# Performance work log

Hardware: AMD Instinct MI355X
Metric: run time of the kernel (lower is better)

Reference implementation:

```python
import jax, jax.numpy as jnp
import numpy as np

VOCAB = 50257
HIDDEN = 2048
BATCH = 8
SEQ = 2048
TOPK = 256


def setup_inputs() -> dict:
    key = jax.random.key(0)
    k1, k2 = jax.random.split(key)
    input_ids = jax.random.randint(k1, (BATCH, SEQ), 0, VOCAB, dtype=jnp.int64)
    W = jax.random.normal(k2, (VOCAB, HIDDEN), dtype=jnp.float32)
    return {"input_ids": input_ids, "W": W, "k": TOPK}


def reference(input_ids, W, k):
    # Embedding gather: [B, S] ids -> [B, S, H] logits (irregular row gather).
    logits = jnp.take(W, input_ids, axis=0)
    # Top-k over the last (hidden) dim, sorted descending (matches torch.topk).
    values, indices = jax.lax.top_k(logits, k)
    return values, indices.astype(jnp.int32)
```

## Files before the change

### kernel.cpp

```cpp
#include <hip/hip_runtime.h>
#include <stdint.h>

#define VOCAB  50257
#define HIDDEN 2048
#define NTOK   (8 * 2048)
#define TOPK   256
#define WPB    4


__device__ __forceinline__ void cmpex(uint64_t& a, uint64_t& b, bool desc) {
    bool gt = a > b;
    uint64_t mx = gt ? a : b;
    uint64_t mn = gt ? b : a;
    a = desc ? mx : mn;
    b = desc ? mn : mx;
}

__device__ __forceinline__ void step_xor(uint64_t& v, int r, int lane, int lx, int k) {
    uint64_t p = __shfl_xor(v, lx, 64);
    int i = lane * 4 + r;
    bool desc = ((i & k) == 0);
    bool low  = ((lane & lx) == 0);
    bool keep_max = (desc == low);
    bool gt = v > p;
    v = (keep_max == gt) ? v : p;
}

__global__ __launch_bounds__(256) void topk_kernel(
    const int* __restrict__ ids,
    const float* __restrict__ W,
    float* __restrict__ out)
{
    const int lane = threadIdx.x & 63;
    const int w    = threadIdx.x >> 6;
    const int row  = blockIdx.x * WPB + w;

    __shared__ uint32_t hist[WPB][256];
    __shared__ __align__(16) uint64_t sel[WPB][256];
    __shared__ uint32_t cnt[WPB];

    const int id = ids[row];
    const float4* src = (const float4*)(W + (size_t)id * HIDDEN);

    uint32_t sv[32];
#pragma unroll
    for (int c = 0; c < 8; ++c) {
        float4 v = src[c * 64 + lane];
        uint32_t u[4] = {__float_as_uint(v.x), __float_as_uint(v.y),
                         __float_as_uint(v.z), __float_as_uint(v.w)};
#pragma unroll
        for (int j = 0; j < 4; ++j) {
            uint32_t m = (u[j] & 0x80000000u) ? 0xFFFFFFFFu : 0x80000000u;
            sv[c * 4 + j] = u[j] ^ m;
        }
    }

    uint32_t active = 0xFFFFFFFFu;
    uint32_t rem    = TOPK;
    uint64_t prefix = 0;
    uint64_t Tkey   = 0;
    bool done = false;

#pragma unroll
    for (int bp = 40; bp >= 0; bp -= 8) {
        if (!done) {
            *(uint4*)&hist[w][lane * 4] = make_uint4(0u, 0u, 0u, 0u);
            __threadfence_block();
#pragma unroll
            for (int e = 0; e < 32; ++e) {
                if (active & (1u << e)) {
                    uint32_t d;
                    if (bp >= 16) {
                        d = (sv[e] >> (bp - 16)) & 0xFFu;
                    } else {
                        uint32_t idx = (uint32_t)((e >> 2) * 256 + lane * 4 + (e & 3));
                        d = ((0xFFFFu ^ idx) >> bp) & 0xFFu;
                    }
                    atomicAdd(&hist[w][d], 1u);
                }
            }
            __threadfence_block();

            uint4 h = *(uint4*)&hist[w][lane * 4];
            uint32_t s3 = h.w;
            uint32_t s2 = h.z + s3;
            uint32_t s1 = h.y + s2;
            uint32_t s0 = h.x + s1;
            uint32_t suf = s0;
#pragma unroll
            for (int off = 1; off < 64; off <<= 1) {
                uint32_t t2 = __shfl_down(suf, off, 64);
                suf += (lane + off < 64) ? t2 : 0u;
            }
            uint32_t above = suf - s0;

            uint32_t dsel = 0, grp = 0, nrem = 0;
            bool found = false;
            uint32_t hm[4] = {h.x, h.y, h.z, h.w};
            uint32_t sm[4] = {s0, s1, s2, s3};
#pragma unroll
            for (int m = 0; m < 4; ++m) {
                uint32_t ge = above + sm[m];
                uint32_t gt = ge - hm[m];
                if (ge >= rem && gt < rem) {
                    found = true;
                    dsel = (uint32_t)(lane * 4 + m);
                    grp  = hm[m];
                    nrem = rem - gt;
                }
            }
            uint64_t ball = __ballot(found);
            int srcl = __builtin_ctzll(ball);
            uint64_t pack = ((uint64_t)dsel << 32) | ((uint64_t)grp << 16) | nrem;
            pack = __shfl(pack, srcl, 64);
            dsel = (uint32_t)(pack >> 32);
            grp  = (uint32_t)((pack >> 16) & 0xFFFFu);
            nrem = (uint32_t)(pack & 0xFFFFu);

            prefix = (prefix << 8) | dsel;
            rem = nrem;
            if (grp == nrem) {
                Tkey = prefix << bp;
                done = true;
            } else {
#pragma unroll
                for (int e = 0; e < 32; ++e) {
                    if (active & (1u << e)) {
                        uint32_t d;
                        if (bp >= 16) {
                            d = (sv[e] >> (bp - 16)) & 0xFFu;
                        } else {
                            uint32_t idx = (uint32_t)((e >> 2) * 256 + lane * 4 + (e & 3));
                            d = ((0xFFFFu ^ idx) >> bp) & 0xFFu;
                        }
                        if (d != dsel) active &= ~(1u << e);
                    }
                }
            }
        }
    }

    if (lane == 0) cnt[w] = 0;
    __threadfence_block();
#pragma unroll
    for (int e = 0; e < 32; ++e) {
        uint32_t idx = (uint32_t)((e >> 2) * 256 + lane * 4 + (e & 3));
        uint64_t kk = ((uint64_t)sv[e] << 16) | (uint64_t)(0xFFFFu ^ idx);
        if (kk >= Tkey) {
            uint32_t p = atomicAdd(&cnt[w], 1u);
            if (p < 256u) sel[w][p] = kk;
        }
    }
    __threadfence_block();

    uint64_t v0 = sel[w][lane * 4 + 0];
    uint64_t v1 = sel[w][lane * 4 + 1];
    uint64_t v2 = sel[w][lane * 4 + 2];
    uint64_t v3 = sel[w][lane * 4 + 3];

#pragma unroll
    for (int k = 2; k <= 256; k <<= 1) {
#pragma unroll
        for (int j = 128; j >= 4; j >>= 1) {
            if (j <= (k >> 1)) {
                int lx = j >> 2;
                step_xor(v0, 0, lane, lx, k);
                step_xor(v1, 1, lane, lx, k);
                step_xor(v2, 2, lane, lx, k);
                step_xor(v3, 3, lane, lx, k);
            }
        }
        if (k >= 4) {
            bool d02 = (((lane * 4 + 0) & k) == 0);
            bool d13 = (((lane * 4 + 1) & k) == 0);
            cmpex(v0, v2, d02);
            cmpex(v1, v3, d13);
        }
        bool d01 = (((lane * 4 + 0) & k) == 0);
        bool d23 = (((lane * 4 + 2) & k) == 0);
        cmpex(v0, v1, d01);
        cmpex(v2, v3, d23);
    }

    uint64_t kk[4] = {v0, v1, v2, v3};
    float ov[4], oi[4];
#pragma unroll
    for (int r = 0; r < 4; ++r) {
        uint32_t s = (uint32_t)(kk[r] >> 16);
        ov[r] = __uint_as_float((s & 0x80000000u) ? (s & 0x7FFFFFFFu) : ~s);
        oi[r] = (float)(0xFFFFu ^ (uint32_t)(kk[r] & 0xFFFFu));
    }
    float4* out_v = (float4*)(out + (size_t)row * TOPK);
    float4* out_i = (float4*)(out + (size_t)NTOK * TOPK + (size_t)row * TOPK);
    out_v[lane] = make_float4(ov[0], ov[1], ov[2], ov[3]);
    out_i[lane] = make_float4(oi[0], oi[1], oi[2], oi[3]);
}

extern "C" void kernel_launch(void* const* d_in, const int* in_sizes, int n_in,
                              void* d_out, int out_size, void* d_ws, size_t ws_size,
                              hipStream_t stream) {
    const int*   ids = (const int*)d_in[0];
    const float* W   = (const float*)d_in[1];
    float* out = (float*)d_out;

    topk_kernel<<<NTOK / WPB, 256, 0, stream>>>(ids, W, out);
}
```

Measured before the change: 535.0 us.

## Replace radix-histogram threshold search with ballot-based binary search on key values

The per-row threshold search drops the shared-memory 8-bit radix histogram with LDS atomics. It now binary-searches the 32-bit sortable key, counting elements at or above each midpoint with wave ballots and popcounts. Ties at the threshold are resolved by ballot-based ranking in index order, and the compaction into the select buffer uses ballot prefix offsets instead of an atomic counter. This removes the LDS atomics and the hist/cnt arrays. In exchange it can take up to 32 search iterations, each scanning all 32 elements with ballots.

```diff
diff --git a/kernel.cpp b/kernel.cpp
--- a/kernel.cpp
+++ b/kernel.cpp
@@ -35,9 +35,7 @@
     const int w    = threadIdx.x >> 6;
     const int row  = blockIdx.x * WPB + w;
 
-    __shared__ uint32_t hist[WPB][256];
     __shared__ __align__(16) uint64_t sel[WPB][256];
-    __shared__ uint32_t cnt[WPB];
 
     const int id = ids[row];
     const float4* src = (const float4*)(W + (size_t)id * HIDDEN);
@@ -55,101 +53,71 @@
         }
     }
 
-    uint32_t active = 0xFFFFFFFFu;
-    uint32_t rem    = TOPK;
-    uint64_t prefix = 0;
-    uint64_t Tkey   = 0;
-    bool done = false;
+    auto count_ge = [&](uint32_t T) -> uint32_t {
+        uint32_t tot = 0;
+#pragma unroll
+        for (int e = 0; e < 32; ++e)
+            tot += (uint32_t)__popcll(__ballot(sv[e] >= T));
+        return tot;
+    };
 
+    uint32_t lo = 0u, hi = 0xFFFFFFFFu;
+    uint32_t Tsel = 0u;
+    bool exact = false;
+    while (lo < hi) {
+        uint32_t mid = lo + ((hi - lo) >> 1) + 1u;
+        uint32_t c = count_ge(mid);
+        if (c == TOPK) { Tsel = mid; exact = true; break; }
+        if (c > TOPK) lo = mid; else hi = mid - 1u;
+    }
+
+    uint32_t selmask = 0u;
+    if (exact) {
 #pragma unroll
-    for (int bp = 40; bp >= 0; bp -= 8) {
-        if (!done) {
-            *(uint4*)&hist[w][lane * 4] = make_uint4(0u, 0u, 0u, 0u);
-            __threadfence_block();
+        for (int e = 0; e < 32; ++e)
+            if (sv[e] >= Tsel) selmask |= (1u << e);
+    } else {
+        uint32_t vstar = lo;
+        uint32_t m = (vstar == 0xFFFFFFFFu) ? 0u : count_ge(vstar + 1u);
+        uint32_t r = TOPK - m;
+        const uint64_t below = (1ull << lane) - 1ull;
+        uint32_t base = 0u;
+        for (int c = 0; c < 8; ++c) {
+            uint64_t bj[4];
+            uint32_t pre = 0u;
 #pragma unroll
-            for (int e = 0; e < 32; ++e) {
-                if (active & (1u << e)) {
-                    uint32_t d;
-                    if (bp >= 16) {
-                        d = (sv[e] >> (bp - 16)) & 0xFFu;
-                    } else {
-                        uint32_t idx = (uint32_t)((e >> 2) * 256 + lane * 4 + (e & 3));
-                        d = ((0xFFFFu ^ idx) >> bp) & 0xFFu;
-                    }
-                    atomicAdd(&hist[w][d], 1u);
-                }
+            for (int j = 0; j < 4; ++j) {
+                bj[j] = __ballot(sv[c * 4 + j] == vstar);
+                pre += (uint32_t)__popcll(bj[j] & below);
             }
-            __threadfence_block();
-
-            uint4 h = *(uint4*)&hist[w][lane * 4];
-            uint32_t s3 = h.w;
-            uint32_t s2 = h.z + s3;
-            uint32_t s1 = h.y + s2;
-            uint32_t s0 = h.x + s1;
-            uint32_t suf = s0;
+            uint32_t ownpref = 0u;
 #pragma unroll
-            for (int off = 1; off < 64; off <<= 1) {
-                uint32_t t2 = __shfl_down(suf, off, 64);
-                suf += (lane + off < 64) ? t2 : 0u;
+            for (int j = 0; j < 4; ++j) {
+                int e = c * 4 + j;
+                bool eq = (sv[e] == vstar);
+                uint32_t rank = base + pre + ownpref;
+                if (sv[e] > vstar || (eq && rank < r)) selmask |= (1u << e);
+                ownpref += eq ? 1u : 0u;
             }
-            uint32_t above = suf - s0;
-
-            uint32_t dsel = 0, grp = 0, nrem = 0;
-            bool found = false;
-            uint32_t hm[4] = {h.x, h.y, h.z, h.w};
-            uint32_t sm[4] = {s0, s1, s2, s3};
 #pragma unroll
-            for (int m = 0; m < 4; ++m) {
-                uint32_t ge = above + sm[m];
-                uint32_t gt = ge - hm[m];
-                if (ge >= rem && gt < rem) {
-                    found = true;
-                    dsel = (uint32_t)(lane * 4 + m);
-                    grp  = hm[m];
-                    nrem = rem - gt;
-                }
-            }
-            uint64_t ball = __ballot(found);
-            int srcl = __builtin_ctzll(ball);
-            uint64_t pack = ((uint64_t)dsel << 32) | ((uint64_t)grp << 16) | nrem;
-            pack = __shfl(pack, srcl, 64);
-            dsel = (uint32_t)(pack >> 32);
-            grp  = (uint32_t)((pack >> 16) & 0xFFFFu);
-            nrem = (uint32_t)(pack & 0xFFFFu);
-
-            prefix = (prefix << 8) | dsel;
-            rem = nrem;
-            if (grp == nrem) {
-                Tkey = prefix << bp;
-                done = true;
-            } else {
-#pragma unroll
-                for (int e = 0; e < 32; ++e) {
-                    if (active & (1u << e)) {
-                        uint32_t d;
-                        if (bp >= 16) {
-                            d = (sv[e] >> (bp - 16)) & 0xFFu;
-                        } else {
-                            uint32_t idx = (uint32_t)((e >> 2) * 256 + lane * 4 + (e & 3));
-                            d = ((0xFFFFu ^ idx) >> bp) & 0xFFu;
-                        }
-                        if (d != dsel) active &= ~(1u << e);
-                    }
-                }
-            }
+            for (int j = 0; j < 4; ++j)
+                base += (uint32_t)__popcll(bj[j]);
         }
     }
 
-    if (lane == 0) cnt[w] = 0;
-    __threadfence_block();
+    const uint64_t below = (1ull << lane) - 1ull;
+    uint32_t pbase = 0u;
 #pragma unroll
     for (int e = 0; e < 32; ++e) {
-        uint32_t idx = (uint32_t)((e >> 2) * 256 + lane * 4 + (e & 3));
-        uint64_t kk = ((uint64_t)sv[e] << 16) | (uint64_t)(0xFFFFu ^ idx);
-        if (kk >= Tkey) {
-            uint32_t p = atomicAdd(&cnt[w], 1u);
-            if (p < 256u) sel[w][p] = kk;
+        bool s = (selmask >> e) & 1u;
+        uint64_t mm = __ballot(s);
+        if (s) {
+            uint32_t idx = (uint32_t)((e >> 2) * 256 + lane * 4 + (e & 3));
+            uint64_t kk = ((uint64_t)sv[e] << 16) | (uint64_t)(0xFFFFu ^ idx);
+            uint32_t p = pbase + (uint32_t)__popcll(mm & below);
+            sel[w][p] = kk;
         }
+        pbase += (uint32_t)__popcll(mm);
     }
     __threadfence_block();
 
```

Result: faster. 515.6 us (-3.6%).
